# Kernel optimization log

Hardware: AMD Instinct MI355X
Metric: run time of the kernel (lower is better)

The kernel has to match this reference:

```python
import jax, jax.numpy as jnp
import numpy as np

B, K, D, H = 16, 256, 256, 128

def setup_inputs() -> dict:
    key = jax.random.key(0)
    k1, k2, k3 = jax.random.split(key, 3)
    x = jax.random.normal(k1, (B, K, D), dtype=jnp.float32)
    # Linear(2D, H): weight stored as (2D, H) for x @ W convention
    W1 = jax.random.normal(k2, (2 * D, H), dtype=jnp.float32) * (1.0 / np.sqrt(2 * D))
    b1 = jnp.zeros((H,), dtype=jnp.float32)
    W2 = jax.random.normal(k3, (H, D), dtype=jnp.float32) * (1.0 / np.sqrt(H))
    b2 = jnp.zeros((D,), dtype=jnp.float32)
    return {"x": x, "W1": W1, "b1": b1, "W2": W2, "b2": b2}

def reference(x, W1, b1, W2, b2):
    # Original: for each i, concat([x_i broadcast, x_j]) -> Linear -> ReLU -> Linear -> mean_j, + residual.
    # Split the first Linear over the concat: W1 = [W1a; W1b], so
    # pre-act(i,j) = x_i @ W1a + x_j @ W1b + b1  (avoids materializing the concat).
    D_ = x.shape[-1]
    W1a, W1b = W1[:D_], W1[D_:]
    a = jnp.einsum('bkd,dh->bkh', x, W1a)            # B x K x H (query side)
    b = jnp.einsum('bkd,dh->bkh', x, W1b)            # B x K x H (key side)
    h = jax.nn.relu(a[:, :, None, :] + b[:, None, :, :] + b1)  # B x K x K x H
    mh = h.mean(axis=2)                               # mean over j; Linear commutes with mean
    out = jnp.einsum('bkh,hd->bkd', mh, W2) + b2      # B x K x D
    return out + x
```

## Files before the change

### kernel.cpp

```cpp
#include <hip/hip_runtime.h>

#define NM 4096
#define NKI 256
#define NH 128
#define ND 256

typedef __attribute__((ext_vector_type(8))) short bf16x8;
typedef __attribute__((ext_vector_type(4))) float f32x4;

__device__ __forceinline__ unsigned short f2bf(float f) {
  unsigned u = __float_as_uint(f);
  u += 0x7FFFu + ((u >> 16) & 1u);
  return (unsigned short)(u >> 16);
}

__global__ __launch_bounds__(256) void k1_mfma(
    const float* __restrict__ x, const float* __restrict__ W1,
    const float* __restrict__ b1, float* __restrict__ GT)
{
  __shared__ unsigned short xs[32 * 256];

  const int tid = threadIdx.x, lane = tid & 63, wu = tid >> 6;
  const int m0 = blockIdx.x * 32;
  const int n0 = blockIdx.y * 64;
  const int fr = lane & 15, fq = lane >> 4;

#pragma unroll
  for (int r = 0; r < 8; ++r) {
    int idx = r * 256 + tid;
    int row = idx >> 6, u = idx & 63;
    float4 v = *(const float4*)&x[(size_t)(m0 + row) * NKI + u * 4];
    ushort4 hv = make_ushort4(f2bf(v.x), f2bf(v.y), f2bf(v.z), f2bf(v.w));
    int pu = u ^ ((row & 7) << 1);
    *(ushort4*)&xs[row * 256 + pu * 4] = hv;
  }

  const int isC = (n0 >= 128);
  const int ncol = (n0 & 127) + wu * 16 + fr;
  const float* __restrict__ wp = W1 + (size_t)(isC ? 256 : 0) * NH + ncol;
  bf16x8 afr[8];
#pragma unroll
  for (int c = 0; c < 8; ++c) {
    union { bf16x8 v; unsigned short s[8]; } t;
#pragma unroll
    for (int j = 0; j < 8; ++j)
      t.s[j] = f2bf(wp[(size_t)(c * 32 + fq * 8 + j) * NH]);
    afr[c] = t.v;
  }
  __syncthreads();

#pragma unroll
  for (int ms = 0; ms < 2; ++ms) {
    f32x4 acc = {0.f, 0.f, 0.f, 0.f};
    const int mrow = ms * 16 + fr;
    const int xsw = (mrow & 7) << 1;
#pragma unroll
    for (int c = 0; c < 8; ++c) {
      int pu = (c * 8 + fq * 2) ^ xsw;
      bf16x8 bfr = *(const bf16x8*)&xs[mrow * 256 + pu * 4];
      acc = __builtin_amdgcn_mfma_f32_16x16x32_bf16(afr[c], bfr, acc, 0, 0, 0);
    }
    const int nb = n0 + wu * 16 + fq * 4;
    const int m = m0 + ms * 16 + fr;
#pragma unroll
    for (int g = 0; g < 4; ++g) {
      float v = acc[g];
      const int nn = nb + g;
      if (nn >= 128) v += b1[nn - 128];
      GT[(size_t)nn * NM + m] = v;
    }
  }
}

__global__ __launch_bounds__(512) void k2a_pair(
    const float* __restrict__ GT, unsigned short* __restrict__ mhb)
{
  __shared__ float Cs[8][256];
  __shared__ unsigned short tl[256][8];

  const int tid = threadIdx.x, lane = tid & 63, wu = tid >> 6;
  const int b = blockIdx.x, hc = blockIdx.y;
  const int h0 = hc * 8;

  {
    int j = tid >> 6, c4 = tid & 63;
    *(float4*)&Cs[j][c4 * 4] =
        *(const float4*)&GT[(size_t)(128 + h0 + j) * NM + b * 256 + c4 * 4];
  }
  const int h = h0 + wu;
  const float* __restrict__ arow = GT + (size_t)h * NM + b * 256;
  const float av0 = arow[lane];
  const float av1 = arow[64 + lane];
  const float av2 = arow[128 + lane];
  const float av3 = arow[192 + lane];
  __syncthreads();

  float4 s4 = *(const float4*)&Cs[wu][lane * 4];
  float sumC = (s4.x + s4.y) + (s4.z + s4.w);
#pragma unroll
  for (int off = 32; off >= 1; off >>= 1) sumC += __shfl_xor(sumC, off, 64);

  float ab0a = 0.f, ab0b = 0.f, ab1a = 0.f, ab1b = 0.f;
  float ab2a = 0.f, ab2b = 0.f, ab3a = 0.f, ab3b = 0.f;
#pragma unroll 8
  for (int u = 0; u < 64; ++u) {
    float4 c = *(const float4*)&Cs[wu][u * 4];
    ab0a += fabsf(av0 + c.x); ab0b += fabsf(av0 + c.y);
    ab0a += fabsf(av0 + c.z); ab0b += fabsf(av0 + c.w);
    ab1a += fabsf(av1 + c.x); ab1b += fabsf(av1 + c.y);
    ab1a += fabsf(av1 + c.z); ab1b += fabsf(av1 + c.w);
    ab2a += fabsf(av2 + c.x); ab2b += fabsf(av2 + c.y);
    ab2a += fabsf(av2 + c.z); ab2b += fabsf(av2 + c.w);
    ab3a += fabsf(av3 + c.x); ab3b += fabsf(av3 + c.y);
    ab3a += fabsf(av3 + c.z); ab3b += fabsf(av3 + c.w);
  }

  tl[lane][wu]       = f2bf((256.f * av0 + sumC + (ab0a + ab0b)) * (1.f / 512.f));
  tl[64 + lane][wu]  = f2bf((256.f * av1 + sumC + (ab1a + ab1b)) * (1.f / 512.f));
  tl[128 + lane][wu] = f2bf((256.f * av2 + sumC + (ab2a + ab2b)) * (1.f / 512.f));
  tl[192 + lane][wu] = f2bf((256.f * av3 + sumC + (ab3a + ab3b)) * (1.f / 512.f));
  __syncthreads();

  if (tid < 256) {
    *(uint4*)&mhb[(size_t)(b * 256 + tid) * NH + h0] =
        *(const uint4*)&tl[tid][0];
  }
}

__global__ __launch_bounds__(256) void k2b_mfma(
    const unsigned short* __restrict__ mhb, const float* __restrict__ W2,
    const float* __restrict__ b2, const float* __restrict__ x,
    float* __restrict__ out)
{
  const int tid = threadIdx.x, lane = tid & 63, wu = tid >> 6;
  const int m0 = blockIdx.x * 32;
  const int d0 = (blockIdx.y * 4 + wu) * 16;
  const int fr = lane & 15, fq = lane >> 4;

  const float* __restrict__ w2p = W2 + d0 + fr;
  bf16x8 bfr[4];
#pragma unroll
  for (int c = 0; c < 4; ++c) {
    union { bf16x8 v; unsigned short s[8]; } t;
#pragma unroll
    for (int j = 0; j < 8; ++j)
      t.s[j] = f2bf(w2p[(size_t)(c * 32 + fq * 8 + j) * ND]);
    bfr[c] = t.v;
  }

  const float bv = b2[d0 + fr];
#pragma unroll
  for (int ms = 0; ms < 2; ++ms) {
    const unsigned short* apm = mhb + (size_t)(m0 + ms * 16 + fr) * NH + fq * 8;
    f32x4 acc = {0.f, 0.f, 0.f, 0.f};
#pragma unroll
    for (int c = 0; c < 4; ++c) {
      bf16x8 a = *(const bf16x8*)(apm + c * 32);
      acc = __builtin_amdgcn_mfma_f32_16x16x32_bf16(a, bfr[c], acc, 0, 0, 0);
    }
#pragma unroll
    for (int g = 0; g < 4; ++g) {
      const int m = m0 + ms * 16 + fq * 4 + g;
      const size_t o = (size_t)m * ND + d0 + fr;
      out[o] = acc[g] + bv + x[o];
    }
  }
}

extern "C" void kernel_launch(void* const* d_in, const int* in_sizes, int n_in,
                              void* d_out, int out_size, void* d_ws, size_t ws_size,
                              hipStream_t stream) {
  const float* x  = (const float*)d_in[0];
  const float* W1 = (const float*)d_in[1];
  const float* b1 = (const float*)d_in[2];
  const float* W2 = (const float*)d_in[3];
  const float* b2 = (const float*)d_in[4];
  float* out = (float*)d_out;

  char* ws = (char*)d_ws;
  float* GT = (float*)ws;
  unsigned short* mhb = (unsigned short*)(ws + (4u << 20));

  k1_mfma<<<dim3(128, 4), 256, 0, stream>>>(x, W1, b1, GT);
  k2a_pair<<<dim3(16, 16), 512, 0, stream>>>(GT, mhb);
  k2b_mfma<<<dim3(128, 4), 256, 0, stream>>>(mhb, W2, b2, x, out);
}
```

Baseline: 26.37 us.

## Fuse first projection into pairwise kernel, keeping A/C activations in LDS

Merges the W1 projection kernel into the pairwise relu-mean kernel. Each block now computes its own 8 query and 8 key hidden columns for one batch directly into shared memory, removing the global GT intermediate and one launch. In exchange, every block reloads and converts the whole 256x256 x slice for its batch, 16x redundant reads. It also needs about 147KB of LDS, which limits occupancy to one block per CU.

```diff
diff --git a/kernel.cpp b/kernel.cpp
--- a/kernel.cpp
+++ b/kernel.cpp
@@ -1,9 +1,9 @@
 #include <hip/hip_runtime.h>
 
 #define NM 4096
-#define NKI 256
 #define NH 128
 #define ND 256
+#define STR 260
 
 typedef __attribute__((ext_vector_type(8))) short bf16x8;
 typedef __attribute__((ext_vector_type(4))) float f32x4;
@@ -14,30 +14,22 @@
   return (unsigned short)(u >> 16);
 }
 
-__global__ __launch_bounds__(256) void k1_mfma(
+__global__ __launch_bounds__(512) void kA(
     const float* __restrict__ x, const float* __restrict__ W1,
-    const float* __restrict__ b1, float* __restrict__ GT)
+    const float* __restrict__ b1, unsigned short* __restrict__ mhb)
 {
-  __shared__ unsigned short xs[32 * 256];
+  __shared__ __align__(16) unsigned char smem[131072 + 2 * 8320];
+  unsigned short* xs = (unsigned short*)smem;
+  float* As = (float*)(smem + 131072);
+  float* Cs = (float*)(smem + 131072 + 8320);
 
   const int tid = threadIdx.x, lane = tid & 63, wu = tid >> 6;
-  const int m0 = blockIdx.x * 32;
-  const int n0 = blockIdx.y * 64;
+  const int b = blockIdx.x, hc = blockIdx.y;
+  const int h0 = hc * 8;
   const int fr = lane & 15, fq = lane >> 4;
 
-#pragma unroll
-  for (int r = 0; r < 8; ++r) {
-    int idx = r * 256 + tid;
-    int row = idx >> 6, u = idx & 63;
-    float4 v = *(const float4*)&x[(size_t)(m0 + row) * NKI + u * 4];
-    ushort4 hv = make_ushort4(f2bf(v.x), f2bf(v.y), f2bf(v.z), f2bf(v.w));
-    int pu = u ^ ((row & 7) << 1);
-    *(ushort4*)&xs[row * 256 + pu * 4] = hv;
-  }
-
-  const int isC = (n0 >= 128);
-  const int ncol = (n0 & 127) + wu * 16 + fr;
-  const float* __restrict__ wp = W1 + (size_t)(isC ? 256 : 0) * NH + ncol;
+  const float* __restrict__ wp =
+      W1 + (size_t)((fr >= 8) ? 256 : 0) * NH + h0 + (fr & 7);
   bf16x8 afr[8];
 #pragma unroll
   for (int c = 0; c < 8; ++c) {
@@ -47,55 +39,53 @@
       t.s[j] = f2bf(wp[(size_t)(c * 32 + fq * 8 + j) * NH]);
     afr[c] = t.v;
   }
+
+#pragma unroll 8
+  for (int i = 0; i < 32; ++i) {
+    const int idx = i * 512 + tid;
+    const int row = idx >> 6, u = idx & 63;
+    float4 v = *(const float4*)&x[(size_t)(b * 256 + row) * 256 + u * 4];
+    ushort4 hv = make_ushort4(f2bf(v.x), f2bf(v.y), f2bf(v.z), f2bf(v.w));
+    *(ushort4*)&xs[row * 256 + (u ^ ((row & 7) << 1)) * 4] = hv;
+  }
   __syncthreads();
 
+  float b1v[4] = {0.f, 0.f, 0.f, 0.f};
+  if (fq >= 2) {
 #pragma unroll
-  for (int ms = 0; ms < 2; ++ms) {
+    for (int g = 0; g < 4; ++g) b1v[g] = b1[h0 + (fq - 2) * 4 + g];
+  }
+
+#pragma unroll
+  for (int ts = 0; ts < 2; ++ts) {
+    const int mrow = (wu * 2 + ts) * 16 + fr;
+    const int swz = (mrow & 7) << 1;
     f32x4 acc = {0.f, 0.f, 0.f, 0.f};
-    const int mrow = ms * 16 + fr;
-    const int xsw = (mrow & 7) << 1;
 #pragma unroll
     for (int c = 0; c < 8; ++c) {
-      int pu = (c * 8 + fq * 2) ^ xsw;
+      const int pu = (c * 8 + fq * 2) ^ swz;
       bf16x8 bfr = *(const bf16x8*)&xs[mrow * 256 + pu * 4];
       acc = __builtin_amdgcn_mfma_f32_16x16x32_bf16(afr[c], bfr, acc, 0, 0, 0);
     }
-    const int nb = n0 + wu * 16 + fq * 4;
-    const int m = m0 + ms * 16 + fr;
+    if (fq < 2) {
 #pragma unroll
-    for (int g = 0; g < 4; ++g) {
-      float v = acc[g];
-      const int nn = nb + g;
-      if (nn >= 128) v += b1[nn - 128];
-      GT[(size_t)nn * NM + m] = v;
+      for (int g = 0; g < 4; ++g) As[(fq * 4 + g) * STR + mrow] = acc[g];
+    } else {
+#pragma unroll
+      for (int g = 0; g < 4; ++g)
+        Cs[((fq - 2) * 4 + g) * STR + mrow] = acc[g] + b1v[g];
     }
   }
-}
-
-__global__ __launch_bounds__(512) void k2a_pair(
-    const float* __restrict__ GT, unsigned short* __restrict__ mhb)
-{
-  __shared__ float Cs[8][256];
-  __shared__ unsigned short tl[256][8];
-
-  const int tid = threadIdx.x, lane = tid & 63, wu = tid >> 6;
-  const int b = blockIdx.x, hc = blockIdx.y;
-  const int h0 = hc * 8;
-
-  {
-    int j = tid >> 6, c4 = tid & 63;
-    *(float4*)&Cs[j][c4 * 4] =
-        *(const float4*)&GT[(size_t)(128 + h0 + j) * NM + b * 256 + c4 * 4];
-  }
-  const int h = h0 + wu;
-  const float* __restrict__ arow = GT + (size_t)h * NM + b * 256;
-  const float av0 = arow[lane];
-  const float av1 = arow[64 + lane];
-  const float av2 = arow[128 + lane];
-  const float av3 = arow[192 + lane];
   __syncthreads();
 
-  float4 s4 = *(const float4*)&Cs[wu][lane * 4];
+  const float* __restrict__ Arow = As + wu * STR;
+  const float* __restrict__ Crow = Cs + wu * STR;
+  const float a0 = Arow[lane];
+  const float a1 = Arow[64 + lane];
+  const float a2 = Arow[128 + lane];
+  const float a3 = Arow[192 + lane];
+
+  float4 s4 = *(const float4*)&Crow[lane * 4];
   float sumC = (s4.x + s4.y) + (s4.z + s4.w);
 #pragma unroll
   for (int off = 32; off >= 1; off >>= 1) sumC += __shfl_xor(sumC, off, 64);
@@ -104,30 +94,38 @@
   float ab2a = 0.f, ab2b = 0.f, ab3a = 0.f, ab3b = 0.f;
 #pragma unroll 8
   for (int u = 0; u < 64; ++u) {
-    float4 c = *(const float4*)&Cs[wu][u * 4];
-    ab0a += fabsf(av0 + c.x); ab0b += fabsf(av0 + c.y);
-    ab0a += fabsf(av0 + c.z); ab0b += fabsf(av0 + c.w);
-    ab1a += fabsf(av1 + c.x); ab1b += fabsf(av1 + c.y);
-    ab1a += fabsf(av1 + c.z); ab1b += fabsf(av1 + c.w);
-    ab2a += fabsf(av2 + c.x); ab2b += fabsf(av2 + c.y);
-    ab2a += fabsf(av2 + c.z); ab2b += fabsf(av2 + c.w);
-    ab3a += fabsf(av3 + c.x); ab3b += fabsf(av3 + c.y);
-    ab3a += fabsf(av3 + c.z); ab3b += fabsf(av3 + c.w);
+    float4 c = *(const float4*)&Crow[u * 4];
+    ab0a += fabsf(a0 + c.x); ab0b += fabsf(a0 + c.y);
+    ab0a += fabsf(a0 + c.z); ab0b += fabsf(a0 + c.w);
+    ab1a += fabsf(a1 + c.x); ab1b += fabsf(a1 + c.y);
+    ab1a += fabsf(a1 + c.z); ab1b += fabsf(a1 + c.w);
+    ab2a += fabsf(a2 + c.x); ab2b += fabsf(a2 + c.y);
+    ab2a += fabsf(a2 + c.z); ab2b += fabsf(a2 + c.w);
+    ab3a += fabsf(a3 + c.x); ab3b += fabsf(a3 + c.y);
+    ab3a += fabsf(a3 + c.z); ab3b += fabsf(a3 + c.w);
   }
 
-  tl[lane][wu]       = f2bf((256.f * av0 + sumC + (ab0a + ab0b)) * (1.f / 512.f));
-  tl[64 + lane][wu]  = f2bf((256.f * av1 + sumC + (ab1a + ab1b)) * (1.f / 512.f));
-  tl[128 + lane][wu] = f2bf((256.f * av2 + sumC + (ab2a + ab2b)) * (1.f / 512.f));
-  tl[192 + lane][wu] = f2bf((256.f * av3 + sumC + (ab3a + ab3b)) * (1.f / 512.f));
+  const float mh0 = (256.f * a0 + sumC + (ab0a + ab0b)) * (1.f / 512.f);
+  const float mh1 = (256.f * a1 + sumC + (ab1a + ab1b)) * (1.f / 512.f);
+  const float mh2 = (256.f * a2 + sumC + (ab2a + ab2b)) * (1.f / 512.f);
+  const float mh3 = (256.f * a3 + sumC + (ab3a + ab3b)) * (1.f / 512.f);
+  __syncthreads();
+
+  As[wu * STR + lane]       = mh0;
+  As[wu * STR + 64 + lane]  = mh1;
+  As[wu * STR + 128 + lane] = mh2;
+  As[wu * STR + 192 + lane] = mh3;
   __syncthreads();
 
   if (tid < 256) {
-    *(uint4*)&mhb[(size_t)(b * 256 + tid) * NH + h0] =
-        *(const uint4*)&tl[tid][0];
+    union { uint4 v; unsigned short s[8]; } o;
+#pragma unroll
+    for (int j = 0; j < 8; ++j) o.s[j] = f2bf(As[j * STR + tid]);
+    *(uint4*)&mhb[(size_t)(b * 256 + tid) * NH + h0] = o.v;
   }
 }
 
-__global__ __launch_bounds__(256) void k2b_mfma(
+__global__ __launch_bounds__(256) void kB_mfma(
     const unsigned short* __restrict__ mhb, const float* __restrict__ W2,
     const float* __restrict__ b2, const float* __restrict__ x,
     float* __restrict__ out)
@@ -177,11 +175,8 @@
   const float* b2 = (const float*)d_in[4];
   float* out = (float*)d_out;
 
-  char* ws = (char*)d_ws;
-  float* GT = (float*)ws;
-  unsigned short* mhb = (unsigned short*)(ws + (4u << 20));
+  unsigned short* mhb = (unsigned short*)d_ws;
 
-  k1_mfma<<<dim3(128, 4), 256, 0, stream>>>(x, W1, b1, GT);
-  k2a_pair<<<dim3(16, 16), 512, 0, stream>>>(GT, mhb);
-  k2b_mfma<<<dim3(128, 4), 256, 0, stream>>>(mhb, W2, b2, x, out);
+  kA<<<dim3(16, 16), 512, 0, stream>>>(x, W1, b1, mhb);
+  kB_mfma<<<dim3(128, 4), 256, 0, stream>>>(mhb, W2, b2, x, out);
 }
```

Measured after the change: 25.25 us. 4.3% less time.
